# Optimization experiments

Measured on AMD Instinct MI355X. Metric: run time of the kernel, lower is better.

The kernel has to match this reference:

```python
import jax, jax.numpy as jnp
from jax import lax
import numpy as np

B = 1024
CH = 32          # decomp.channel
LEVEL = 3        # decomp.level
CTOT = CH * (LEVEL + 1)   # 128, ODE state dim == GRU input dim
T_POINTS = 96    # decomp.eval_time_points
PRED_LEN = 96
HID = 128


def _dopri5_traj(y0, ts, Wo, bo):
    """Fixed-grid Dormand-Prince 5(4) integration of dy/dt = tanh(y Wo^T + bo).
    y0: [B, CTOT]; ts: [T]. Returns trajectory [T, B, CTOT]."""
    f = lambda y: jnp.tanh(y @ Wo.T + bo)

    def step(y, dt):
        k1 = f(y)
        k2 = f(y + dt * (0.2 * k1))
        k3 = f(y + dt * (3.0 / 40 * k1 + 9.0 / 40 * k2))
        k4 = f(y + dt * (44.0 / 45 * k1 - 56.0 / 15 * k2 + 32.0 / 9 * k3))
        k5 = f(y + dt * (19372.0 / 6561 * k1 - 25360.0 / 2187 * k2 + 64448.0 / 6561 * k3 - 212.0 / 729 * k4))
        k6 = f(y + dt * (9017.0 / 3168 * k1 - 355.0 / 33 * k2 + 46732.0 / 5247 * k3 + 49.0 / 176 * k4 - 5103.0 / 18656 * k5))
        y_next = y + dt * (35.0 / 384 * k1 + 500.0 / 1113 * k3 + 125.0 / 192 * k4 - 2187.0 / 6784 * k5 + 11.0 / 84 * k6)
        return y_next, y_next

    _, ys = lax.scan(step, y0, ts[1:] - ts[:-1])
    return jnp.concatenate([y0[None], ys], axis=0)


def _gru_layer(xs, W_ih, W_hh, b_ih, b_hh):
    """PyTorch-semantics GRU layer. xs: [T, B, D] -> hidden states [T, B, H]."""
    gi = jnp.einsum('tbd,gd->tbg', xs, W_ih) + b_ih  # precompute input gates
    H = W_hh.shape[1]

    def cell(h, gi_t):
        gh = h @ W_hh.T + b_hh
        i_r, i_z, i_n = jnp.split(gi_t, 3, axis=-1)
        h_r, h_z, h_n = jnp.split(gh, 3, axis=-1)
        r = jax.nn.sigmoid(i_r + h_r)
        z = jax.nn.sigmoid(i_z + h_z)
        n = jnp.tanh(i_n + r * h_n)
        h_new = (1.0 - z) * n + z * h
        return h_new, h_new

    h0 = jnp.zeros((xs.shape[1], H), xs.dtype)
    _, hs = lax.scan(cell, h0, gi)
    return hs


def setup_inputs() -> dict:
    key = jax.random.key(0)
    ks = jax.random.split(key, 20)
    s = 0.08  # ~1/sqrt(128), keeps GRU/ODE in a stable regime
    return {
        'x': jax.random.normal(ks[0], (B, CH, 256), jnp.float32),
        'yl': jax.random.normal(ks[1], (B, CH, 1), jnp.float32),
        'yh': jax.random.normal(ks[2], (B, CH * LEVEL, 1), jnp.float32),
        'W_ode': jax.random.normal(ks[3], (CTOT, CTOT), jnp.float32) * 0.05,
        'b_ode': jax.random.normal(ks[4], (CTOT,), jnp.float32) * 0.05,
        'W_ih0': jax.random.normal(ks[5], (3 * HID, CTOT), jnp.float32) * s,
        'W_hh0': jax.random.normal(ks[6], (3 * HID, HID), jnp.float32) * s,
        'b_ih0': jax.random.normal(ks[7], (3 * HID,), jnp.float32) * s,
        'b_hh0': jax.random.normal(ks[8], (3 * HID,), jnp.float32) * s,
        'W_ih1': jax.random.normal(ks[9], (3 * HID, HID), jnp.float32) * s,
        'W_hh1': jax.random.normal(ks[10], (3 * HID, HID), jnp.float32) * s,
        'b_ih1': jax.random.normal(ks[11], (3 * HID,), jnp.float32) * s,
        'b_hh1': jax.random.normal(ks[12], (3 * HID,), jnp.float32) * s,
        'W1': jax.random.normal(ks[13], (64, HID), jnp.float32) * s,
        'b1': jax.random.normal(ks[14], (64,), jnp.float32) * s,
        'W2': jax.random.normal(ks[15], (PRED_LEN * CH, 64), jnp.float32) * 0.125,
        'b2': jax.random.normal(ks[16], (PRED_LEN * CH,), jnp.float32) * 0.125,
    }


def reference(x, yl, yh, W_ode, b_ode,
              W_ih0, W_hh0, b_ih0, b_hh0,
              W_ih1, W_hh1, b_ih1, b_hh1,
              W1, b1, W2, b2):
    # coeffs = cat([yl] + yh, dim=1) -> [B, CTOT, 1] -> squeeze coeff length (=1)
    coeffs = jnp.concatenate([yl, yh], axis=1)[..., 0]  # [B, CTOT]
    ts = jnp.linspace(0.0, 1.0, T_POINTS)
    traj = _dopri5_traj(coeffs, ts, W_ode, b_ode)  # [T, B, CTOT]
    # rearrange 't b c l -> b t (c l)' with l == 1; GRU scans over leading T axis
    h1 = _gru_layer(traj, W_ih0, W_hh0, b_ih0, b_hh0)   # [T, B, HID]
    h2 = _gru_layer(h1, W_ih1, W_hh1, b_ih1, b_hh1)     # [T, B, HID]
    last = h2[-1]                                        # [B, HID]
    hidden = jax.nn.gelu(last @ W1.T + b1, approximate=False)
    pred = hidden @ W2.T + b2                            # [B, PRED_LEN*CH]
    return pred.reshape(-1, CH, PRED_LEN)
```

## Files before the change

### kernel.cpp

```cpp
#include <hip/hip_runtime.h>
#include <hip/hip_bf16.h>
#include <math.h>

#define TPTS 96
#define CTOT 128
#define LDP 134

typedef __bf16 bf16x8_t __attribute__((ext_vector_type(8)));
typedef float f32x4_t __attribute__((ext_vector_type(4)));
typedef unsigned short us8_t __attribute__((ext_vector_type(8)));

__device__ __forceinline__ unsigned short f2b(float f) {
    union { float f; unsigned int i; } v; v.f = f;
    unsigned int r = v.i + 0x7fffu + ((v.i >> 16) & 1u);
    return (unsigned short)(r >> 16);
}
__device__ __forceinline__ unsigned int packbf2(float a, float b) {
    unsigned int r;
    asm("v_cvt_pk_bf16_f32 %0, %1, %2" : "=v"(r) : "v"(a), "v"(b));
    return r;
}
__device__ __forceinline__ uint2 pack4(float v0, float v1, float v2, float v3) {
    uint2 w; w.x = packbf2(v0, v1); w.y = packbf2(v2, v3); return w;
}
__device__ __forceinline__ f32x4_t mfma16(bf16x8_t a, bf16x8_t b, f32x4_t c) {
    return __builtin_amdgcn_mfma_f32_16x16x32_bf16(a, b, c, 0, 0, 0);
}
__device__ __forceinline__ bf16x8_t ldfrag(const unsigned short* p) {
    us8_t v = *(const us8_t*)p;
    return __builtin_bit_cast(bf16x8_t, v);
}
__device__ __forceinline__ bf16x8_t ldfragG(const unsigned short* p) {
    union { unsigned long long q[2]; us8_t v; } u;
    u.q[0] = __hip_atomic_load((const unsigned long long*)p,
                               __ATOMIC_RELAXED, __HIP_MEMORY_SCOPE_AGENT);
    u.q[1] = __hip_atomic_load((const unsigned long long*)(p + 4),
                               __ATOMIC_RELAXED, __HIP_MEMORY_SCOPE_AGENT);
    return __builtin_bit_cast(bf16x8_t, u.v);
}
__device__ __forceinline__ void stg8(unsigned short* p, uint2 pk) {
    unsigned long long q = ((unsigned long long)pk.y << 32) | (unsigned long long)pk.x;
    __hip_atomic_store((unsigned long long*)p, q,
                       __ATOMIC_RELAXED, __HIP_MEMORY_SCOPE_AGENT);
}
__device__ __forceinline__ bf16x8_t ldfragW(const float* p) {
    float4 a = *(const float4*)p;
    float4 b = *(const float4*)(p + 4);
    bf16x8_t r;
    r[0] = __builtin_bit_cast(__bf16, f2b(a.x)); r[1] = __builtin_bit_cast(__bf16, f2b(a.y));
    r[2] = __builtin_bit_cast(__bf16, f2b(a.z)); r[3] = __builtin_bit_cast(__bf16, f2b(a.w));
    r[4] = __builtin_bit_cast(__bf16, f2b(b.x)); r[5] = __builtin_bit_cast(__bf16, f2b(b.y));
    r[6] = __builtin_bit_cast(__bf16, f2b(b.z)); r[7] = __builtin_bit_cast(__bf16, f2b(b.w));
    return r;
}
__device__ __forceinline__ float tanh2(float x) {
    float e = __expf(x + x);
    return 1.f - __fdividef(2.f, e + 1.f);
}
__device__ __forceinline__ float sigm(float x) {
    return __fdividef(1.f, 1.f + __expf(-x));
}

#define LGKM_BAR() do {                                         \
        asm volatile("s_waitcnt lgkmcnt(0)" ::: "memory");      \
        __builtin_amdgcn_s_barrier();                           \
    } while (0)

__device__ __forceinline__ void waitflag(unsigned int* f, unsigned int want) {
    if (threadIdx.x == 0) {
        int guard = 0;
        while (__hip_atomic_load(f, __ATOMIC_RELAXED, __HIP_MEMORY_SCOPE_AGENT) != want) {
            __builtin_amdgcn_s_sleep(1);
            if (++guard > (1 << 22)) break;
        }
    }
    __syncthreads();
}
__device__ __forceinline__ void setflag(unsigned int* f, unsigned int val) {
    if (threadIdx.x == 0) {
        asm volatile("s_waitcnt vmcnt(0)" ::: "memory");
        __hip_atomic_store(f, val, __ATOMIC_RELAXED, __HIP_MEMORY_SCOPE_AGENT);
    }
}

__global__ void __launch_bounds__(512, 2)
ode_forecaster(const float* __restrict__ yl,
               const float* __restrict__ yh,
               const float* __restrict__ Wode,
               const float* __restrict__ bode,
               const float* __restrict__ Wih0,
               const float* __restrict__ Whh0,
               const float* __restrict__ bih0,
               const float* __restrict__ bhh0,
               const float* __restrict__ Wih1,
               const float* __restrict__ Whh1,
               const float* __restrict__ bih1,
               const float* __restrict__ bhh1,
               const float* __restrict__ W1v,
               const float* __restrict__ b1v,
               const float* __restrict__ W2v,
               const float* __restrict__ b2v,
               float* __restrict__ outp,
               char* __restrict__ wsb)
{
    const int role = blockIdx.x >> 6;
    const int c    = blockIdx.x & 63;
    const int tid  = threadIdx.x, lane = tid & 63, wv = tid >> 6;
    const int l15  = lane & 15, quad = lane >> 4;
    const int fbase = wv * 16 + quad * 4;
    const int rbase = c * 16;

    __shared__ __align__(16) unsigned short zbuf[2][16][LDP];
    __shared__ __align__(16) unsigned short hidbuf[16][72];

    unsigned short* yTraj  = (unsigned short*)(wsb);
    unsigned short* h1Traj = (unsigned short*)(wsb + 0x2000000);
    unsigned int*   yflag  = (unsigned int*)(wsb + 0x4000000);
    unsigned int*   h1flag = (unsigned int*)(wsb + 0x4010000);
#define YMAGIC(t)  (0x5E000000u + (unsigned)(t))
#define H1MAGIC(t) (0x6E000000u + (unsigned)(t))

    if (role == 0) {
        bf16x8_t wode[4];
#pragma unroll
        for (int kt = 0; kt < 4; ++kt)
            wode[kt] = ldfragW(Wode + (wv * 16 + l15) * CTOT + kt * 32 + quad * 8);
        float bo2[4];
        {
            float4 b4 = *(const float4*)(bode + fbase);
            bo2[0] = 2.f * b4.x; bo2[1] = 2.f * b4.y; bo2[2] = 2.f * b4.z; bo2[3] = 2.f * b4.w;
        }
        float y[4];
        {
            int row = rbase + l15;
#pragma unroll
            for (int i = 0; i < 4; ++i) {
                int f = fbase + i;
                y[i] = (f < 32) ? yl[row * 32 + f] : yh[row * 96 + (f - 32)];
            }
            uint2 pk = pack4(y[0], y[1], y[2], y[3]);
            *(uint2*)&zbuf[0][l15][fbase] = pk;
            stg8(yTraj + ((size_t)row) * CTOT + fbase, pk);
        }
        __syncthreads();
        setflag(&yflag[c * 128 + 0], YMAGIC(0));

        const float dt = 1.0f / 95.0f;
        const float d10 = dt * 0.2f;
        const float d20 = dt * (3.f/40.f),  d21 = dt * (9.f/40.f);
        const float d30 = dt * (44.f/45.f), d31 = dt * (-56.f/15.f), d32 = dt * (32.f/9.f);
        const float d40 = dt * (19372.f/6561.f), d41 = dt * (-25360.f/2187.f),
                    d42 = dt * (64448.f/6561.f), d43 = dt * (-212.f/729.f);
        const float d50 = dt * (9017.f/3168.f), d51 = dt * (-355.f/33.f),
                    d52 = dt * (46732.f/5247.f), d53 = dt * (49.f/176.f),
                    d54 = dt * (-5103.f/18656.f);
        const float e0 = dt * (35.f/384.f), e2 = dt * (500.f/1113.f), e3 = dt * (125.f/192.f),
                    e4 = dt * (-2187.f/6784.f), e5 = dt * (11.f/84.f);

        int p = 0;
        float kr[6][4];
#pragma unroll 1
        for (int t = 0; t < 95; ++t) {
#pragma unroll
            for (int s = 0; s < 6; ++s) {
                bf16x8_t bf[4];
#pragma unroll
                for (int kt = 0; kt < 4; ++kt)
                    bf[kt] = ldfrag(&zbuf[p][l15][kt * 32 + quad * 8]);
                const f32x4_t zz = {0.f, 0.f, 0.f, 0.f};
                f32x4_t a0 = mfma16(wode[0], bf[0], zz);
                f32x4_t a1 = mfma16(wode[1], bf[1], zz);
                f32x4_t a2 = mfma16(wode[2], bf[2], zz);
                f32x4_t a3 = mfma16(wode[3], bf[3], zz);
                f32x4_t acc = (a0 + a1) + (a2 + a3);
#pragma unroll
                for (int i = 0; i < 4; ++i) {
                    float e = __expf(fmaf(acc[i], 2.f, bo2[i]));
                    kr[s][i] = 1.f - __fdividef(2.f, e + 1.f);
                }

                if (s < 5) {
                    float z[4];
#pragma unroll
                    for (int i = 0; i < 4; ++i) {
                        float zv;
                        if (s == 0)      zv = y[i] + d10 * kr[0][i];
                        else if (s == 1) zv = y[i] + d20 * kr[0][i] + d21 * kr[1][i];
                        else if (s == 2) zv = y[i] + d30 * kr[0][i] + d31 * kr[1][i] + d32 * kr[2][i];
                        else if (s == 3) zv = y[i] + d40 * kr[0][i] + d41 * kr[1][i]
                                             + d42 * kr[2][i] + d43 * kr[3][i];
                        else             zv = y[i] + d50 * kr[0][i] + d51 * kr[1][i]
                                             + d52 * kr[2][i] + d53 * kr[3][i] + d54 * kr[4][i];
                        z[i] = zv;
                    }
                    *(uint2*)&zbuf[p ^ 1][l15][fbase] = pack4(z[0], z[1], z[2], z[3]);
                } else {
#pragma unroll
                    for (int i = 0; i < 4; ++i)
                        y[i] += e0*kr[0][i] + e2*kr[2][i] + e3*kr[3][i] + e4*kr[4][i] + e5*kr[5][i];
                    uint2 pk = pack4(y[0], y[1], y[2], y[3]);
                    *(uint2*)&zbuf[p ^ 1][l15][fbase] = pk;
                    stg8(yTraj + ((size_t)(t + 1) * 1024 + rbase + l15) * CTOT + fbase, pk);
                }
                if (s == 1)
                    asm volatile("s_waitcnt vmcnt(0)" ::: "memory");
                LGKM_BAR();
                if (s == 1 && t > 0 && tid == 0)
                    __hip_atomic_store(&yflag[c * 128 + t], YMAGIC(t),
                                       __ATOMIC_RELAXED, __HIP_MEMORY_SCOPE_AGENT);
                p ^= 1;
            }
        }
        asm volatile("s_waitcnt vmcnt(0)" ::: "memory");
        __builtin_amdgcn_s_barrier();
        if (tid == 0)
            __hip_atomic_store(&yflag[c * 128 + 95], YMAGIC(95),
                               __ATOMIC_RELAXED, __HIP_MEMORY_SCOPE_AGENT);
        return;
    }

    const float* Wih = (role == 1) ? Wih0 : Wih1;
    const float* Whh = (role == 1) ? Whh0 : Whh1;
    const float* bih = (role == 1) ? bih0 : bih1;
    const float* bhh = (role == 1) ? bhh0 : bhh1;
    const unsigned short* src = (role == 1) ? yTraj : h1Traj;
    unsigned int* sflag = (role == 1) ? yflag : h1flag;

    bf16x8_t wih[3][4], whh[3][4];
#pragma unroll
    for (int g = 0; g < 3; ++g)
#pragma unroll
        for (int kt = 0; kt < 4; ++kt) {
            wih[g][kt] = ldfragW(Wih + (size_t)(g * 128 + wv * 16 + l15) * CTOT + kt * 32 + quad * 8);
            whh[g][kt] = ldfragW(Whh + (size_t)(g * 128 + wv * 16 + l15) * CTOT + kt * 32 + quad * 8);
        }
    float br[4], bz[4], bin_[4], bhn[4];
    {
        float4 a0 = *(const float4*)(bih + 0 * 128 + fbase);
        float4 b0 = *(const float4*)(bhh + 0 * 128 + fbase);
        float4 a1 = *(const float4*)(bih + 1 * 128 + fbase);
        float4 b1 = *(const float4*)(bhh + 1 * 128 + fbase);
        float4 a2 = *(const float4*)(bih + 2 * 128 + fbase);
        float4 b2 = *(const float4*)(bhh + 2 * 128 + fbase);
        br[0] = a0.x + b0.x; br[1] = a0.y + b0.y; br[2] = a0.z + b0.z; br[3] = a0.w + b0.w;
        bz[0] = a1.x + b1.x; bz[1] = a1.y + b1.y; bz[2] = a1.z + b1.z; bz[3] = a1.w + b1.w;
        bin_[0] = a2.x; bin_[1] = a2.y; bin_[2] = a2.z; bin_[3] = a2.w;
        bhn[0] = b2.x; bhn[1] = b2.y; bhn[2] = b2.z; bhn[3] = b2.w;
    }

    float h[4] = {0.f, 0.f, 0.f, 0.f};
    *(uint2*)&zbuf[0][l15][fbase] = pack4(0.f, 0.f, 0.f, 0.f);
    int p = 0;
    __syncthreads();

    if (role == 1) {
#pragma unroll 1
        for (int t = 0; t < TPTS; ++t) {
            asm volatile("s_waitcnt vmcnt(0)" ::: "memory");
            __builtin_amdgcn_s_barrier();
            if (tid == 0) {
                if (t > 0)
                    __hip_atomic_store(&h1flag[c * 128 + (t - 1)], H1MAGIC(t - 1),
                                       __ATOMIC_RELAXED, __HIP_MEMORY_SCOPE_AGENT);
                int guard = 0;
                while (__hip_atomic_load(&yflag[c * 128 + t],
                                         __ATOMIC_RELAXED, __HIP_MEMORY_SCOPE_AGENT) != YMAGIC(t)) {
                    __builtin_amdgcn_s_sleep(1);
                    if (++guard > (1 << 22)) break;
                }
            }
            __syncthreads();
            const unsigned short* xp = src + ((size_t)t * 1024 + rbase + l15) * CTOT;
            bf16x8_t ax[4], ah[4];
#pragma unroll
            for (int kt = 0; kt < 4; ++kt) {
                ax[kt] = ldfragG(xp + kt * 32 + quad * 8);
                ah[kt] = ldfrag(&zbuf[p][l15][kt * 32 + quad * 8]);
            }
            f32x4_t gx[3], gh[3];
#pragma unroll
            for (int g = 0; g < 3; ++g) {
                gx[g] = (f32x4_t){0.f, 0.f, 0.f, 0.f};
                gh[g] = (f32x4_t){0.f, 0.f, 0.f, 0.f};
            }
#pragma unroll
            for (int kt = 0; kt < 4; ++kt) {
                gx[0] = mfma16(wih[0][kt], ax[kt], gx[0]);
                gx[1] = mfma16(wih[1][kt], ax[kt], gx[1]);
                gx[2] = mfma16(wih[2][kt], ax[kt], gx[2]);
                gh[0] = mfma16(whh[0][kt], ah[kt], gh[0]);
                gh[1] = mfma16(whh[1][kt], ah[kt], gh[1]);
                gh[2] = mfma16(whh[2][kt], ah[kt], gh[2]);
            }
#pragma unroll
            for (int i = 0; i < 4; ++i) {
                float rr = sigm(gx[0][i] + gh[0][i] + br[i]);
                float zz = sigm(gx[1][i] + gh[1][i] + bz[i]);
                float nn = tanh2((gx[2][i] + bin_[i]) + rr * (gh[2][i] + bhn[i]));
                h[i] = nn + zz * (h[i] - nn);
            }
            uint2 pk = pack4(h[0], h[1], h[2], h[3]);
            *(uint2*)&zbuf[p ^ 1][l15][fbase] = pk;
            stg8(h1Traj + ((size_t)t * 1024 + rbase + l15) * CTOT + fbase, pk);
            LGKM_BAR();
            p ^= 1;
        }
        asm volatile("s_waitcnt vmcnt(0)" ::: "memory");
        __syncthreads();
        if (tid == 0)
            __hip_atomic_store(&h1flag[c * 128 + (TPTS - 1)], H1MAGIC(TPTS - 1),
                               __ATOMIC_RELAXED, __HIP_MEMORY_SCOPE_AGENT);
        return;
    }

#pragma unroll 1
    for (int t = 0; t < TPTS; ++t) {
        waitflag(&sflag[c * 128 + t], H1MAGIC(t));
        const unsigned short* xp = src + ((size_t)t * 1024 + rbase + l15) * CTOT;
        bf16x8_t ax[4], ah[4];
#pragma unroll
        for (int kt = 0; kt < 4; ++kt) {
            ax[kt] = ldfragG(xp + kt * 32 + quad * 8);
            ah[kt] = ldfrag(&zbuf[p][l15][kt * 32 + quad * 8]);
        }
        f32x4_t gx[3], gh[3];
#pragma unroll
        for (int g = 0; g < 3; ++g) {
            gx[g] = (f32x4_t){0.f, 0.f, 0.f, 0.f};
            gh[g] = (f32x4_t){0.f, 0.f, 0.f, 0.f};
        }
#pragma unroll
        for (int kt = 0; kt < 4; ++kt) {
            gx[0] = mfma16(wih[0][kt], ax[kt], gx[0]);
            gx[1] = mfma16(wih[1][kt], ax[kt], gx[1]);
            gx[2] = mfma16(wih[2][kt], ax[kt], gx[2]);
            gh[0] = mfma16(whh[0][kt], ah[kt], gh[0]);
            gh[1] = mfma16(whh[1][kt], ah[kt], gh[1]);
            gh[2] = mfma16(whh[2][kt], ah[kt], gh[2]);
        }
#pragma unroll
        for (int i = 0; i < 4; ++i) {
            float rr = sigm(gx[0][i] + gh[0][i] + br[i]);
            float zz = sigm(gx[1][i] + gh[1][i] + bz[i]);
            float nn = tanh2((gx[2][i] + bin_[i]) + rr * (gh[2][i] + bhn[i]));
            h[i] = nn + zz * (h[i] - nn);
        }
        *(uint2*)&zbuf[p ^ 1][l15][fbase] = pack4(h[0], h[1], h[2], h[3]);
        LGKM_BAR();
        p ^= 1;
    }

    if (wv < 4) {
        bf16x8_t wf[4], hf[4];
#pragma unroll
        for (int kt = 0; kt < 4; ++kt) {
            wf[kt] = ldfragW(W1v + (size_t)(wv * 16 + l15) * CTOT + kt * 32 + quad * 8);
            hf[kt] = ldfrag(&zbuf[p][l15][kt * 32 + quad * 8]);
        }
        f32x4_t acc = {0.f, 0.f, 0.f, 0.f};
#pragma unroll
        for (int kt = 0; kt < 4; ++kt) acc = mfma16(wf[kt], hf[kt], acc);
        float4 bb = *(const float4*)(b1v + wv * 16 + quad * 4);
        const float* bbp = (const float*)&bb;
        float gl[4];
#pragma unroll
        for (int i = 0; i < 4; ++i) {
            float x = acc[i] + bbp[i];
            gl[i] = 0.5f * x * (1.0f + erff(x * 0.70710678118654752f));
        }
        *(uint2*)&hidbuf[l15][wv * 16 + quad * 4] = pack4(gl[0], gl[1], gl[2], gl[3]);
    }
    __syncthreads();

    bf16x8_t ahid[2];
#pragma unroll
    for (int kt = 0; kt < 2; ++kt)
        ahid[kt] = ldfrag(&hidbuf[l15][kt * 32 + quad * 8]);
#pragma unroll 1
    for (int j = 0; j < 24; ++j) {
        int mt2 = wv * 24 + j;
        bf16x8_t wf0 = ldfragW(W2v + (size_t)(mt2 * 16 + l15) * 64 + quad * 8);
        bf16x8_t wf1 = ldfragW(W2v + (size_t)(mt2 * 16 + l15) * 64 + 32 + quad * 8);
        float4 bv = *(const float4*)(b2v + mt2 * 16 + quad * 4);
        const float* bvp = (const float*)&bv;
        f32x4_t acc = {0.f, 0.f, 0.f, 0.f};
        acc = mfma16(wf0, ahid[0], acc);
        acc = mfma16(wf1, ahid[1], acc);
        float4 o;
        o.x = acc[0] + bvp[0]; o.y = acc[1] + bvp[1];
        o.z = acc[2] + bvp[2]; o.w = acc[3] + bvp[3];
        *(float4*)(outp + (size_t)(rbase + l15) * 3072 + mt2 * 16 + quad * 4) = o;
    }
#undef YMAGIC
#undef H1MAGIC
}

extern "C" void kernel_launch(void* const* d_in, const int* in_sizes, int n_in,
                              void* d_out, int out_size, void* d_ws, size_t ws_size,
                              hipStream_t stream) {
    const float* yl   = (const float*)d_in[1];
    const float* yh   = (const float*)d_in[2];
    const float* Wode = (const float*)d_in[3];
    const float* bode = (const float*)d_in[4];
    const float* Wih0 = (const float*)d_in[5];
    const float* Whh0 = (const float*)d_in[6];
    const float* bih0 = (const float*)d_in[7];
    const float* bhh0 = (const float*)d_in[8];
    const float* Wih1 = (const float*)d_in[9];
    const float* Whh1 = (const float*)d_in[10];
    const float* bih1 = (const float*)d_in[11];
    const float* bhh1 = (const float*)d_in[12];
    const float* W1v  = (const float*)d_in[13];
    const float* b1v  = (const float*)d_in[14];
    const float* W2v  = (const float*)d_in[15];
    const float* b2v  = (const float*)d_in[16];

    ode_forecaster<<<dim3(192), dim3(512), 0, stream>>>(
        yl, yh, Wode, bode, Wih0, Whh0, bih0, bhh0,
        Wih1, Whh1, bih1, bhh1, W1v, b1v, W2v, b2v,
        (float*)d_out, (char*)d_ws);
}
```

Before: 764.3 us.

## Run ODE stage on single wave with LDS weights, hoist recurrent GRU matmul before flag wait

The ODE producer block now stages the bf16 ODE weight matrix in LDS and runs the whole Dormand-Prince step on one wavefront. Each wave computes all 128 outputs for its 16 rows, which removes the per-stage block barriers. Intermediate k values are kept as packed bf16 registers, and tanh uses exp2/rcp intrinsics. In both GRU consumer roles, the hidden-to-hidden MFMAs are issued before waiting on the producer flag, so that work overlaps the dependency wait. Launch bounds drop to one block per CU, and the single-wave ODE does 8x more MFMA work serially per wave, trading parallelism for no synchronisation.

```diff
diff --git a/kernel.cpp b/kernel.cpp
--- a/kernel.cpp
+++ b/kernel.cpp
@@ -5,6 +5,7 @@
 #define TPTS 96
 #define CTOT 128
 #define LDP 134
+#define WP  134
 
 typedef __bf16 bf16x8_t __attribute__((ext_vector_type(8)));
 typedef float f32x4_t __attribute__((ext_vector_type(4)));
@@ -22,6 +23,12 @@
 }
 __device__ __forceinline__ uint2 pack4(float v0, float v1, float v2, float v3) {
     uint2 w; w.x = packbf2(v0, v1); w.y = packbf2(v2, v3); return w;
+}
+__device__ __forceinline__ float upk_lo(unsigned int w) {
+    return __builtin_bit_cast(float, w << 16);
+}
+__device__ __forceinline__ float upk_hi(unsigned int w) {
+    return __builtin_bit_cast(float, w & 0xffff0000u);
 }
 __device__ __forceinline__ f32x4_t mfma16(bf16x8_t a, bf16x8_t b, f32x4_t c) {
     return __builtin_amdgcn_mfma_f32_16x16x32_bf16(a, b, c, 0, 0, 0);
@@ -57,6 +64,12 @@
     float e = __expf(x + x);
     return 1.f - __fdividef(2.f, e + 1.f);
 }
+#define TWO_LOG2E 2.8853900817779268f
+__device__ __forceinline__ float tanhfast(float acc, float bl) {
+    float e = __builtin_amdgcn_exp2f(fmaf(acc, TWO_LOG2E, bl));
+    float r = __builtin_amdgcn_rcpf(e + 1.f);
+    return fmaf(-2.f, r, 1.f);
+}
 __device__ __forceinline__ float sigm(float x) {
     return __fdividef(1.f, 1.f + __expf(-x));
 }
@@ -76,14 +89,8 @@
     }
     __syncthreads();
 }
-__device__ __forceinline__ void setflag(unsigned int* f, unsigned int val) {
-    if (threadIdx.x == 0) {
-        asm volatile("s_waitcnt vmcnt(0)" ::: "memory");
-        __hip_atomic_store(f, val, __ATOMIC_RELAXED, __HIP_MEMORY_SCOPE_AGENT);
-    }
-}
-
-__global__ void __launch_bounds__(512, 2)
+
+__global__ void __launch_bounds__(512, 1)
 ode_forecaster(const float* __restrict__ yl,
                const float* __restrict__ yh,
                const float* __restrict__ Wode,
@@ -112,6 +119,9 @@
 
     __shared__ __align__(16) unsigned short zbuf[2][16][LDP];
     __shared__ __align__(16) unsigned short hidbuf[16][72];
+    __shared__ __align__(16) unsigned short wodeb[128][WP];
+    __shared__ __align__(16) unsigned short zb[16][WP];
+    __shared__ __align__(16) float bolb[128];
 
     unsigned short* yTraj  = (unsigned short*)(wsb);
     unsigned short* h1Traj = (unsigned short*)(wsb + 0x2000000);
@@ -121,29 +131,41 @@
 #define H1MAGIC(t) (0x6E000000u + (unsigned)(t))
 
     if (role == 0) {
-        bf16x8_t wode[4];
-#pragma unroll
-        for (int kt = 0; kt < 4; ++kt)
-            wode[kt] = ldfragW(Wode + (wv * 16 + l15) * CTOT + kt * 32 + quad * 8);
-        float bo2[4];
         {
-            float4 b4 = *(const float4*)(bode + fbase);
-            bo2[0] = 2.f * b4.x; bo2[1] = 2.f * b4.y; bo2[2] = 2.f * b4.z; bo2[3] = 2.f * b4.w;
-        }
-        float y[4];
-        {
-            int row = rbase + l15;
-#pragma unroll
-            for (int i = 0; i < 4; ++i) {
-                int f = fbase + i;
-                y[i] = (f < 32) ? yl[row * 32 + f] : yh[row * 96 + (f - 32)];
-            }
-            uint2 pk = pack4(y[0], y[1], y[2], y[3]);
-            *(uint2*)&zbuf[0][l15][fbase] = pk;
-            stg8(yTraj + ((size_t)row) * CTOT + fbase, pk);
+            int r = tid >> 2, c0 = (tid & 3) * 32;
+            const float* wrow = Wode + r * CTOT + c0;
+#pragma unroll
+            for (int u = 0; u < 32; u += 8) {
+                float4 a = *(const float4*)(wrow + u);
+                float4 b = *(const float4*)(wrow + u + 4);
+                *(uint2*)&wodeb[r][c0 + u]     = pack4(a.x, a.y, a.z, a.w);
+                *(uint2*)&wodeb[r][c0 + u + 4] = pack4(b.x, b.y, b.z, b.w);
+            }
+            if (tid < 128) bolb[tid] = bode[tid] * TWO_LOG2E;
+        }
+
+        const int row = rbase + l15;
+        float y[8][4], yn[8][4];
+        if (wv == 0) {
+#pragma unroll
+            for (int j = 0; j < 8; ++j) {
+#pragma unroll
+                for (int i = 0; i < 4; ++i) {
+                    int f = j * 16 + quad * 4 + i;
+                    y[j][i] = (f < 32) ? yl[row * 32 + f] : yh[row * 96 + (f - 32)];
+                }
+                uint2 pk = pack4(y[j][0], y[j][1], y[j][2], y[j][3]);
+                *(uint2*)&zb[l15][j * 16 + quad * 4] = pk;
+                stg8(yTraj + ((size_t)row) * CTOT + j * 16 + quad * 4, pk);
+            }
         }
         __syncthreads();
-        setflag(&yflag[c * 128 + 0], YMAGIC(0));
+        if (wv != 0) return;
+
+        asm volatile("s_waitcnt vmcnt(0)" ::: "memory");
+        if (lane == 0)
+            __hip_atomic_store(&yflag[c * 128 + 0], YMAGIC(0),
+                               __ATOMIC_RELAXED, __HIP_MEMORY_SCOPE_AGENT);
 
         const float dt = 1.0f / 95.0f;
         const float d10 = dt * 0.2f;
@@ -157,63 +179,90 @@
         const float e0 = dt * (35.f/384.f), e2 = dt * (500.f/1113.f), e3 = dt * (125.f/192.f),
                     e4 = dt * (-2187.f/6784.f), e5 = dt * (11.f/84.f);
 
-        int p = 0;
-        float kr[6][4];
+        unsigned int kp[5][8][2];
+
 #pragma unroll 1
         for (int t = 0; t < 95; ++t) {
 #pragma unroll
             for (int s = 0; s < 6; ++s) {
-                bf16x8_t bf[4];
+                bf16x8_t zf[4];
 #pragma unroll
                 for (int kt = 0; kt < 4; ++kt)
-                    bf[kt] = ldfrag(&zbuf[p][l15][kt * 32 + quad * 8]);
-                const f32x4_t zz = {0.f, 0.f, 0.f, 0.f};
-                f32x4_t a0 = mfma16(wode[0], bf[0], zz);
-                f32x4_t a1 = mfma16(wode[1], bf[1], zz);
-                f32x4_t a2 = mfma16(wode[2], bf[2], zz);
-                f32x4_t a3 = mfma16(wode[3], bf[3], zz);
-                f32x4_t acc = (a0 + a1) + (a2 + a3);
-#pragma unroll
-                for (int i = 0; i < 4; ++i) {
-                    float e = __expf(fmaf(acc[i], 2.f, bo2[i]));
-                    kr[s][i] = 1.f - __fdividef(2.f, e + 1.f);
-                }
-
+                    zf[kt] = ldfrag(&zb[l15][kt * 32 + quad * 8]);
+                float bl[8][4];
+#pragma unroll
+                for (int j = 0; j < 8; ++j) {
+                    float4 bv = *(const float4*)&bolb[j * 16 + quad * 4];
+                    bl[j][0] = bv.x; bl[j][1] = bv.y; bl[j][2] = bv.z; bl[j][3] = bv.w;
+                }
+                f32x4_t acc[8];
+#pragma unroll
+                for (int j = 0; j < 8; ++j) {
+                    acc[j] = (f32x4_t){0.f, 0.f, 0.f, 0.f};
+#pragma unroll
+                    for (int kt = 0; kt < 4; ++kt)
+                        acc[j] = mfma16(ldfrag(&wodeb[j * 16 + l15][kt * 32 + quad * 8]),
+                                        zf[kt], acc[j]);
+                }
+                float kf[8][4];
+#pragma unroll
+                for (int j = 0; j < 8; ++j)
+#pragma unroll
+                    for (int i = 0; i < 4; ++i)
+                        kf[j][i] = tanhfast(acc[j][i], bl[j][i]);
                 if (s < 5) {
-                    float z[4];
+#pragma unroll
+                    for (int j = 0; j < 8; ++j) {
+                        kp[s][j][0] = packbf2(kf[j][0], kf[j][1]);
+                        kp[s][j][1] = packbf2(kf[j][2], kf[j][3]);
+                    }
+                }
+#pragma unroll
+                for (int j = 0; j < 8; ++j)
 #pragma unroll
                     for (int i = 0; i < 4; ++i) {
-                        float zv;
-                        if (s == 0)      zv = y[i] + d10 * kr[0][i];
-                        else if (s == 1) zv = y[i] + d20 * kr[0][i] + d21 * kr[1][i];
-                        else if (s == 2) zv = y[i] + d30 * kr[0][i] + d31 * kr[1][i] + d32 * kr[2][i];
-                        else if (s == 3) zv = y[i] + d40 * kr[0][i] + d41 * kr[1][i]
-                                             + d42 * kr[2][i] + d43 * kr[3][i];
-                        else             zv = y[i] + d50 * kr[0][i] + d51 * kr[1][i]
-                                             + d52 * kr[2][i] + d53 * kr[3][i] + d54 * kr[4][i];
-                        z[i] = zv;
+                        if (s == 0)      yn[j][i] = fmaf(e0, kf[j][i], y[j][i]);
+                        else if (s == 2) yn[j][i] = fmaf(e2, kf[j][i], yn[j][i]);
+                        else if (s == 3) yn[j][i] = fmaf(e3, kf[j][i], yn[j][i]);
+                        else if (s == 4) yn[j][i] = fmaf(e4, kf[j][i], yn[j][i]);
+                        else if (s == 5) y[j][i]  = fmaf(e5, kf[j][i], yn[j][i]);
                     }
-                    *(uint2*)&zbuf[p ^ 1][l15][fbase] = pack4(z[0], z[1], z[2], z[3]);
-                } else {
-#pragma unroll
-                    for (int i = 0; i < 4; ++i)
-                        y[i] += e0*kr[0][i] + e2*kr[2][i] + e3*kr[3][i] + e4*kr[4][i] + e5*kr[5][i];
-                    uint2 pk = pack4(y[0], y[1], y[2], y[3]);
-                    *(uint2*)&zbuf[p ^ 1][l15][fbase] = pk;
-                    stg8(yTraj + ((size_t)(t + 1) * 1024 + rbase + l15) * CTOT + fbase, pk);
-                }
-                if (s == 1)
+#pragma unroll
+                for (int j = 0; j < 8; ++j) {
+                    float zv[4];
+#pragma unroll
+                    for (int i = 0; i < 4; ++i) {
+                        unsigned int h = i >> 1;
+                        float k0 = (i & 1) ? upk_hi(kp[0][j][h]) : upk_lo(kp[0][j][h]);
+                        float k1 = (i & 1) ? upk_hi(kp[1][j][h]) : upk_lo(kp[1][j][h]);
+                        float k2 = (i & 1) ? upk_hi(kp[2][j][h]) : upk_lo(kp[2][j][h]);
+                        float k3 = (i & 1) ? upk_hi(kp[3][j][h]) : upk_lo(kp[3][j][h]);
+                        float zvv;
+                        if (s == 0)      zvv = fmaf(d10, kf[j][i], y[j][i]);
+                        else if (s == 1) zvv = y[j][i] + d20 * k0 + d21 * kf[j][i];
+                        else if (s == 2) zvv = y[j][i] + d30 * k0 + d31 * k1 + d32 * kf[j][i];
+                        else if (s == 3) zvv = y[j][i] + d40 * k0 + d41 * k1
+                                             + d42 * k2 + d43 * kf[j][i];
+                        else if (s == 4) zvv = y[j][i] + d50 * k0 + d51 * k1
+                                             + d52 * k2 + d53 * k3 + d54 * kf[j][i];
+                        else             zvv = y[j][i];
+                        zv[i] = zvv;
+                    }
+                    uint2 pk = pack4(zv[0], zv[1], zv[2], zv[3]);
+                    *(uint2*)&zb[l15][j * 16 + quad * 4] = pk;
+                    if (s == 5)
+                        stg8(yTraj + ((size_t)(t + 1) * 1024 + row) * CTOT + j * 16 + quad * 4, pk);
+                }
+                if (s == 2) {
                     asm volatile("s_waitcnt vmcnt(0)" ::: "memory");
-                LGKM_BAR();
-                if (s == 1 && t > 0 && tid == 0)
-                    __hip_atomic_store(&yflag[c * 128 + t], YMAGIC(t),
-                                       __ATOMIC_RELAXED, __HIP_MEMORY_SCOPE_AGENT);
-                p ^= 1;
+                    if (lane == 0)
+                        __hip_atomic_store(&yflag[c * 128 + t], YMAGIC(t),
+                                           __ATOMIC_RELAXED, __HIP_MEMORY_SCOPE_AGENT);
+                }
             }
         }
         asm volatile("s_waitcnt vmcnt(0)" ::: "memory");
-        __builtin_amdgcn_s_barrier();
-        if (tid == 0)
+        if (lane == 0)
             __hip_atomic_store(&yflag[c * 128 + 95], YMAGIC(95),
                                __ATOMIC_RELAXED, __HIP_MEMORY_SCOPE_AGENT);
         return;
@@ -224,7 +273,6 @@
     const float* bih = (role == 1) ? bih0 : bih1;
     const float* bhh = (role == 1) ? bhh0 : bhh1;
     const unsigned short* src = (role == 1) ? yTraj : h1Traj;
-    unsigned int* sflag = (role == 1) ? yflag : h1flag;
 
     bf16x8_t wih[3][4], whh[3][4];
 #pragma unroll
@@ -256,6 +304,19 @@
     if (role == 1) {
 #pragma unroll 1
         for (int t = 0; t < TPTS; ++t) {
+            bf16x8_t ah[4];
+#pragma unroll
+            for (int kt = 0; kt < 4; ++kt)
+                ah[kt] = ldfrag(&zbuf[p][l15][kt * 32 + quad * 8]);
+            f32x4_t gh[3];
+#pragma unroll
+            for (int g = 0; g < 3; ++g) gh[g] = (f32x4_t){0.f, 0.f, 0.f, 0.f};
+#pragma unroll
+            for (int kt = 0; kt < 4; ++kt) {
+                gh[0] = mfma16(whh[0][kt], ah[kt], gh[0]);
+                gh[1] = mfma16(whh[1][kt], ah[kt], gh[1]);
+                gh[2] = mfma16(whh[2][kt], ah[kt], gh[2]);
+            }
             asm volatile("s_waitcnt vmcnt(0)" ::: "memory");
             __builtin_amdgcn_s_barrier();
             if (tid == 0) {
@@ -271,26 +332,17 @@
             }
             __syncthreads();
             const unsigned short* xp = src + ((size_t)t * 1024 + rbase + l15) * CTOT;
-            bf16x8_t ax[4], ah[4];
-#pragma unroll
-            for (int kt = 0; kt < 4; ++kt) {
-                ax[kt] = ldfragG(xp + kt * 32 + quad * 8);
-                ah[kt] = ldfrag(&zbuf[p][l15][kt * 32 + quad * 8]);
-            }
-            f32x4_t gx[3], gh[3];
-#pragma unroll
-            for (int g = 0; g < 3; ++g) {
-                gx[g] = (f32x4_t){0.f, 0.f, 0.f, 0.f};
-                gh[g] = (f32x4_t){0.f, 0.f, 0.f, 0.f};
-            }
+            bf16x8_t ax[4];
+#pragma unroll
+            for (int kt = 0; kt < 4; ++kt) ax[kt] = ldfragG(xp + kt * 32 + quad * 8);
+            f32x4_t gx[3];
+#pragma unroll
+            for (int g = 0; g < 3; ++g) gx[g] = (f32x4_t){0.f, 0.f, 0.f, 0.f};
 #pragma unroll
             for (int kt = 0; kt < 4; ++kt) {
                 gx[0] = mfma16(wih[0][kt], ax[kt], gx[0]);
                 gx[1] = mfma16(wih[1][kt], ax[kt], gx[1]);
                 gx[2] = mfma16(wih[2][kt], ax[kt], gx[2]);
-                gh[0] = mfma16(whh[0][kt], ah[kt], gh[0]);
-                gh[1] = mfma16(whh[1][kt], ah[kt], gh[1]);
-                gh[2] = mfma16(whh[2][kt], ah[kt], gh[2]);
             }
 #pragma unroll
             for (int i = 0; i < 4; ++i) {
@@ -315,28 +367,32 @@
 
 #pragma unroll 1
     for (int t = 0; t < TPTS; ++t) {
-        waitflag(&sflag[c * 128 + t], H1MAGIC(t));
+        bf16x8_t ah[4];
+#pragma unroll
+        for (int kt = 0; kt < 4; ++kt)
+            ah[kt] = ldfrag(&zbuf[p][l15][kt * 32 + quad * 8]);
+        f32x4_t gh[3];
+#pragma unroll
+        for (int g = 0; g < 3; ++g) gh[g] = (f32x4_t){0.f, 0.f, 0.f, 0.f};
+#pragma unroll
+        for (int kt = 0; kt < 4; ++kt) {
+            gh[0] = mfma16(whh[0][kt], ah[kt], gh[0]);
+            gh[1] = mfma16(whh[1][kt], ah[kt], gh[1]);
+            gh[2] = mfma16(whh[2][kt], ah[kt], gh[2]);
+        }
+        waitflag(&h1flag[c * 128 + t], H1MAGIC(t));
         const unsigned short* xp = src + ((size_t)t * 1024 + rbase + l15) * CTOT;
-        bf16x8_t ax[4], ah[4];
-#pragma unroll
-        for (int kt = 0; kt < 4; ++kt) {
-            ax[kt] = ldfragG(xp + kt * 32 + quad * 8);
-            ah[kt] = ldfrag(&zbuf[p][l15][kt * 32 + quad * 8]);
-        }
-        f32x4_t gx[3], gh[3];
-#pragma unroll
-        for (int g = 0; g < 3; ++g) {
-            gx[g] = (f32x4_t){0.f, 0.f, 0.f, 0.f};
-            gh[g] = (f32x4_t){0.f, 0.f, 0.f, 0.f};
-        }
+        bf16x8_t ax[4];
+#pragma unroll
+        for (int kt = 0; kt < 4; ++kt) ax[kt] = ldfragG(xp + kt * 32 + quad * 8);
+        f32x4_t gx[3];
+#pragma unroll
+        for (int g = 0; g < 3; ++g) gx[g] = (f32x4_t){0.f, 0.f, 0.f, 0.f};
 #pragma unroll
         for (int kt = 0; kt < 4; ++kt) {
             gx[0] = mfma16(wih[0][kt], ax[kt], gx[0]);
             gx[1] = mfma16(wih[1][kt], ax[kt], gx[1]);
             gx[2] = mfma16(wih[2][kt], ax[kt], gx[2]);
-            gh[0] = mfma16(whh[0][kt], ah[kt], gh[0]);
-            gh[1] = mfma16(whh[1][kt], ah[kt], gh[1]);
-            gh[2] = mfma16(whh[2][kt], ah[kt], gh[2]);
         }
 #pragma unroll
         for (int i = 0; i < 4; ++i) {
```

Result: slower. 2.430 ms (+217.9%).
